# Kernel tuning notes

Hardware: AMD Instinct MI355X
Metric: run time of the kernel (lower is better)

The kernel has to match this reference:

```python
import jax, jax.numpy as jnp
import numpy as np

# Static module config (from Encoder's CropConv layers)
B, CIN, COUT, H, W = 32, 256, 256, 64, 64
K, STRIDE, PAD, DIL = 3, 2, 1, 1
OVERLAP, CENTER = 0, 4


def _build_crop_mask(in_h, out_h, out_w, center_size, overlap):
    """Faithful replica of CropConv's python-loop mask construction,
    including python-slice clamping to L = out_h*out_w."""
    L = out_h * out_w
    crop_start = (in_h - in_h // center_size) // 2 - overlap
    start_idx = in_h * crop_start + crop_start
    crop_size = in_h // center_size + overlap * 2
    not_cropped = crop_start * 2

    def seg_len(a, b):
        # length of python slice [a:b] on an array of length L
        return max(0, min(b, L) - min(a, L))

    segs = []
    for i in range(crop_size):
        if i == 0:
            segs.append(np.ones(seg_len(0, start_idx), bool))
        if i == crop_size - 1:
            segs.append(np.zeros(seg_len(start_idx, start_idx + crop_size), bool))
            segs.append(np.ones(seg_len(start_idx + crop_size, in_h * in_h), bool))
            break
        segs.append(np.zeros(seg_len(start_idx, start_idx + crop_size), bool))
        segs.append(np.ones(seg_len(start_idx + crop_size, start_idx + not_cropped), bool))
        start_idx += in_h
    mask = np.concatenate(segs)
    assert mask.shape[0] == L, (mask.shape[0], L)
    return mask.reshape(out_h, out_w)


def setup_inputs() -> dict:
    key = jax.random.key(0)
    kx, kw = jax.random.split(key)
    x = jax.random.normal(kx, (B, CIN, H, W), dtype=jnp.float32)
    # kaiming_normal(mode='fan_out', nonlinearity='relu'): std = sqrt(2 / (COUT*K*K))
    std = np.sqrt(2.0 / (COUT * K * K)).astype(np.float32)
    weight = jax.random.normal(kw, (COUT, CIN, K, K), dtype=jnp.float32) * std
    return {"x": x, "weight": weight}


def reference(x, weight):
    out_h = (H - K + 2 * PAD) // STRIDE + 1
    out_w = (W - K + 2 * PAD) // STRIDE + 1
    # unfold + matmul == standard convolution; use the efficient fused form
    out = jax.lax.conv_general_dilated(
        x, weight,
        window_strides=(STRIDE, STRIDE),
        padding=[(PAD, PAD), (PAD, PAD)],
        rhs_dilation=(DIL, DIL),
        dimension_numbers=("NCHW", "OIHW", "NCHW"))  # [B, COUT, out_h, out_w]
    mask = jnp.asarray(_build_crop_mask(H, out_h, out_w, CENTER, OVERLAP))
    return jnp.where(mask[None, None, :, :], out, jnp.float32(0.0))
```

## Files before the change

### kernel.cpp

```cpp
#include <hip/hip_runtime.h>


#define B_   32
#define CIN  256
#define COUT 256
#define H_   64
#define W_   64
#define OH   32
#define OW   32

typedef _Float16 f16;
typedef _Float16 half8 __attribute__((ext_vector_type(8)));
typedef float    floatx16 __attribute__((ext_vector_type(16)));

__global__ __launch_bounds__(256) void repack_w_kernel(const float* __restrict__ w,
                                                       f16* __restrict__ rp) {
  int o = blockIdx.x * 256 + threadIdx.x;
  int ci_l = o & 15;
  int tt = o >> 4;
  int co_l = tt & 127; tt >>= 7;
  int khw = tt % 9;    tt /= 9;
  int cc   = tt & 15;  tt >>= 4;
  int co_t = tt;
  int co = co_t * 128 + co_l;
  int ci = cc * 16 + ci_l;
  rp[o] = (f16)w[(co * CIN + ci) * 9 + khw];
}

static __device__ __forceinline__ void wg_barrier() {
  __builtin_amdgcn_sched_barrier(0);
  asm volatile("s_waitcnt lgkmcnt(0)" ::: "memory");
  __builtin_amdgcn_s_barrier();
  __builtin_amdgcn_sched_barrier(0);
}

__global__ __launch_bounds__(256, 2) void conv_mfma_kernel(
    const float* __restrict__ x, const f16* __restrict__ rp,
    float* __restrict__ out) {
  __shared__ __align__(16) f16 xs[19040];

  const int t    = threadIdx.x;
  const int lane = t & 63;
  const int wave = t >> 6;
  const int wm   = wave >> 1;
  const int wn   = wave & 1;

  const int blk  = blockIdx.x;
  const int b    = blk >> 4;
  const int rem  = blk & 15;
  const int co_t = rem >> 3;
  const int oh0  = (rem & 7) << 2;
  const int ih0  = 2 * oh0 - 1;

  const float* xb = x + (size_t)b * CIN * H_ * W_;

  const int iw  = t & 63;
  const int rru = __builtin_amdgcn_readfirstlane(t >> 6);
  const int k0  = (lane >> 5) * 8;
  const int ml  = lane & 31;
  const int p_st   = iw & 1;
  const int idx_st = (iw + p_st) >> 1;
  const int gx     = (idx_st >> 3) & 1;

  f16* const xs0 = xs;
  f16* const xs1 = xs + 9520;

  const f16* const AbL = rp + (size_t)co_t * (16 * 9 * 128 * 16)
                            + (wm * 64 + ml) * 16 + k0;

  floatx16 acc[2][2];
#pragma unroll
  for (int mi = 0; mi < 2; ++mi)
#pragma unroll
    for (int nj = 0; nj < 2; ++nj)
#pragma unroll
      for (int i = 0; i < 16; ++i) acc[mi][nj][i] = 0.f;

  float xv[3][2][8];

  auto load_x = [&](const float* bcc) {
#pragma unroll
    for (int it = 0; it < 3; ++it) {
      const int r = rru + it * 4;
      if (r < 9) {
        const int ih = ih0 + r;
        if (ih >= 0) {
          const float* p0 = bcc + (size_t)ih * 64 + iw;
#pragma unroll
          for (int g = 0; g < 2; ++g)
#pragma unroll
            for (int c = 0; c < 8; ++c)
              xv[it][g][c] = p0[(size_t)(g * 8 + c) * 4096];
        } else {
#pragma unroll
          for (int g = 0; g < 2; ++g)
#pragma unroll
            for (int c = 0; c < 8; ++c) xv[it][g][c] = 0.f;
        }
      }
    }
  };

  auto write_x = [&](f16* xoth) {
    f16* d = xoth + p_st * 4760 + idx_st * 16;
#pragma unroll
    for (int it = 0; it < 3; ++it) {
      const int r = rru + it * 4;
      if (r < 9) {
#pragma unroll
        for (int g = 0; g < 2; ++g) {
          half8 v;
#pragma unroll
          for (int c = 0; c < 8; ++c) v[c] = (f16)xv[it][g][c];
          *(half8*)&d[r * 528 + (g ^ gx) * 8] = v;
        }
      }
    }
  };

  auto compute = [&](const f16* Abc, const f16* xcur) {
    half8 a0[9], a1[9];
#pragma unroll
    for (int khw = 0; khw < 9; ++khw) {
      a0[khw] = *(const half8*)&Abc[khw * 2048];
      a1[khw] = *(const half8*)&Abc[khw * 2048 + 512];
    }
    const f16* Be  = xcur + wn * 2112 + ml * 16 + (k0 ^ (ml & 8));
    const f16* Bo1 = Be + 4760;
    const f16* Bo2 = xcur + 4760 + wn * 2112 + (ml + 1) * 16 + (k0 ^ ((ml + 1) & 8));
    __builtin_amdgcn_s_setprio(1);
#pragma unroll
    for (int kh = 0; kh < 3; ++kh) {
#pragma unroll
      for (int kw = 0; kw < 3; ++kw) {
        const int khw = kh * 3 + kw;
        const f16* Bp = (kw == 0) ? Bo1 : (kw == 1) ? Be : Bo2;
#pragma unroll
        for (int nj = 0; nj < 2; ++nj) {
          half8 bf = *(const half8*)&Bp[nj * 1056 + kh * 528];
          acc[0][nj] = __builtin_amdgcn_mfma_f32_32x32x16_f16(a0[khw], bf, acc[0][nj], 0, 0, 0);
          acc[1][nj] = __builtin_amdgcn_mfma_f32_32x32x16_f16(a1[khw], bf, acc[1][nj], 0, 0, 0);
        }
      }
    }
    __builtin_amdgcn_s_setprio(0);
  };

  if (t < 144) {
    const int r = t >> 4, ci = t & 15;
    xs0[4760 + r * 528 + ci] = (f16)0.f;
    xs1[4760 + r * 528 + ci] = (f16)0.f;
  }

  load_x(xb);
  write_x(xs0);
  load_x(xb + 65536);
  __syncthreads();

  const f16* Abc = AbL;
  f16* curp = xs0;
  f16* othp = xs1;
#pragma unroll 1
  for (int cc = 0; cc < 16; ++cc) {
    compute(Abc, curp);
    Abc += 18432;
    if (cc < 15) {
      write_x(othp);
      if (cc < 14) load_x(xb + (size_t)(cc + 2) * 65536);
      wg_barrier();
      f16* tm = curp; curp = othp; othp = tm;
    }
  }

  const int col = ml;
  const int rowbase = (lane >> 5) * 4;
  float* ob = out + ((size_t)b * COUT + co_t * 128 + wm * 64) * (OH * OW);
#pragma unroll
  for (int mi = 0; mi < 2; ++mi) {
#pragma unroll
    for (int nj = 0; nj < 2; ++nj) {
      const int oh = oh0 + wn * 2 + nj;
#pragma unroll
      for (int r = 0; r < 16; ++r) {
        const int row = mi * 32 + (r & 3) + 8 * (r >> 2) + rowbase;
        ob[(size_t)row * (OH * OW) + oh * OW + col] = acc[mi][nj][r];
      }
    }
  }
}

extern "C" void kernel_launch(void* const* d_in, const int* in_sizes, int n_in,
                              void* d_out, int out_size, void* d_ws, size_t ws_size,
                              hipStream_t stream) {
  const float* x = (const float*)d_in[0];
  const float* w = (const float*)d_in[1];
  float* out = (float*)d_out;
  f16* rp = (f16*)d_ws;

  repack_w_kernel<<<2304, 256, 0, stream>>>(w, rp);
  conv_mfma_kernel<<<512, 256, 0, stream>>>(x, rp, out);
}
```

Baseline: 227.9 us.

## Halve output-row tile per block to double grid and raise occupancy

Each block now covers 2 output rows instead of 4, so the grid doubles to 1024 blocks and the per-block LDS input tile shrinks. Accumulators drop to two MFMA tiles per wave, and the A fragments are loaded per kh instead of all nine up front. Launch bounds go to 4 blocks per CU. The aim is more resident waves to hide latency and better CU balance. The cost is reloading weight fragments for twice as many blocks, redundant input halo rows, and half the MFMA work per weight load.

```diff
diff --git a/kernel.cpp b/kernel.cpp
--- a/kernel.cpp
+++ b/kernel.cpp
@@ -34,10 +34,14 @@
   __builtin_amdgcn_sched_barrier(0);
 }
 
-__global__ __launch_bounds__(256, 2) void conv_mfma_kernel(
+#define PLANE 2640
+#define ODD   2648
+#define XBUF  5288
+
+__global__ __launch_bounds__(256, 4) void conv_mfma_kernel(
     const float* __restrict__ x, const f16* __restrict__ rp,
     float* __restrict__ out) {
-  __shared__ __align__(16) f16 xs[19040];
+  __shared__ __align__(16) f16 xs[2 * XBUF];
 
   const int t    = threadIdx.x;
   const int lane = t & 63;
@@ -46,110 +50,99 @@
   const int wn   = wave & 1;
 
   const int blk  = blockIdx.x;
-  const int b    = blk >> 4;
-  const int rem  = blk & 15;
-  const int co_t = rem >> 3;
-  const int oh0  = (rem & 7) << 2;
-  const int ih0  = 2 * oh0 - 1;
+  const int b    = blk >> 5;
+  const int rem  = blk & 31;
+  const int co_t = rem >> 4;
+  const int ohp  = rem & 15;
+  const int oh0  = ohp << 1;
+  const int ih0  = (ohp << 2) - 1;
 
   const float* xb = x + (size_t)b * CIN * H_ * W_;
 
-  const int iw  = t & 63;
-  const int rru = __builtin_amdgcn_readfirstlane(t >> 6);
-  const int k0  = (lane >> 5) * 8;
-  const int ml  = lane & 31;
+  const int iw    = t & 63;
+  const int g_st  = (t >> 6) & 1;
+  const int rbase = __builtin_amdgcn_readfirstlane(t >> 7) * 3;
+  const int k0 = (lane >> 5) * 8;
+  const int ml = lane & 31;
   const int p_st   = iw & 1;
   const int idx_st = (iw + p_st) >> 1;
   const int gx     = (idx_st >> 3) & 1;
 
   f16* const xs0 = xs;
-  f16* const xs1 = xs + 9520;
+  f16* const xs1 = xs + XBUF;
 
   const f16* const AbL = rp + (size_t)co_t * (16 * 9 * 128 * 16)
                             + (wm * 64 + ml) * 16 + k0;
 
-  floatx16 acc[2][2];
+  floatx16 acc[2];
 #pragma unroll
   for (int mi = 0; mi < 2; ++mi)
 #pragma unroll
-    for (int nj = 0; nj < 2; ++nj)
-#pragma unroll
-      for (int i = 0; i < 16; ++i) acc[mi][nj][i] = 0.f;
+    for (int i = 0; i < 16; ++i) acc[mi][i] = 0.f;
 
-  float xv[3][2][8];
+  float xv[3][8];
 
   auto load_x = [&](const float* bcc) {
 #pragma unroll
     for (int it = 0; it < 3; ++it) {
-      const int r = rru + it * 4;
-      if (r < 9) {
+      const int r = rbase + it;
+      if (r < 5) {
         const int ih = ih0 + r;
         if (ih >= 0) {
-          const float* p0 = bcc + (size_t)ih * 64 + iw;
+          const float* p0 = bcc + (size_t)(g_st * 8) * 4096 + (size_t)ih * 64 + iw;
 #pragma unroll
-          for (int g = 0; g < 2; ++g)
-#pragma unroll
-            for (int c = 0; c < 8; ++c)
-              xv[it][g][c] = p0[(size_t)(g * 8 + c) * 4096];
+          for (int c = 0; c < 8; ++c) xv[it][c] = p0[(size_t)c * 4096];
         } else {
 #pragma unroll
-          for (int g = 0; g < 2; ++g)
-#pragma unroll
-            for (int c = 0; c < 8; ++c) xv[it][g][c] = 0.f;
+          for (int c = 0; c < 8; ++c) xv[it][c] = 0.f;
         }
       }
     }
   };
 
   auto write_x = [&](f16* xoth) {
-    f16* d = xoth + p_st * 4760 + idx_st * 16;
+    f16* d = xoth + p_st * ODD + idx_st * 16 + (g_st ^ gx) * 8;
 #pragma unroll
     for (int it = 0; it < 3; ++it) {
-      const int r = rru + it * 4;
-      if (r < 9) {
+      const int r = rbase + it;
+      if (r < 5) {
+        half8 v;
 #pragma unroll
-        for (int g = 0; g < 2; ++g) {
-          half8 v;
-#pragma unroll
-          for (int c = 0; c < 8; ++c) v[c] = (f16)xv[it][g][c];
-          *(half8*)&d[r * 528 + (g ^ gx) * 8] = v;
-        }
+        for (int c = 0; c < 8; ++c) v[c] = (f16)xv[it][c];
+        *(half8*)&d[r * 528] = v;
       }
     }
   };
 
   auto compute = [&](const f16* Abc, const f16* xcur) {
-    half8 a0[9], a1[9];
-#pragma unroll
-    for (int khw = 0; khw < 9; ++khw) {
-      a0[khw] = *(const half8*)&Abc[khw * 2048];
-      a1[khw] = *(const half8*)&Abc[khw * 2048 + 512];
-    }
-    const f16* Be  = xcur + wn * 2112 + ml * 16 + (k0 ^ (ml & 8));
-    const f16* Bo1 = Be + 4760;
-    const f16* Bo2 = xcur + 4760 + wn * 2112 + (ml + 1) * 16 + (k0 ^ ((ml + 1) & 8));
+    const f16* Be  = xcur + wn * 1056 + ml * 16 + (k0 ^ (ml & 8));
+    const f16* Bo1 = Be + ODD;
+    const f16* Bo2 = xcur + ODD + wn * 1056 + (ml + 1) * 16 + (k0 ^ ((ml + 1) & 8));
     __builtin_amdgcn_s_setprio(1);
 #pragma unroll
     for (int kh = 0; kh < 3; ++kh) {
+      half8 a0[3], a1[3];
 #pragma unroll
       for (int kw = 0; kw < 3; ++kw) {
-        const int khw = kh * 3 + kw;
+        a0[kw] = *(const half8*)&Abc[(kh * 3 + kw) * 2048];
+        a1[kw] = *(const half8*)&Abc[(kh * 3 + kw) * 2048 + 512];
+      }
+#pragma unroll
+      for (int kw = 0; kw < 3; ++kw) {
         const f16* Bp = (kw == 0) ? Bo1 : (kw == 1) ? Be : Bo2;
-#pragma unroll
-        for (int nj = 0; nj < 2; ++nj) {
-          half8 bf = *(const half8*)&Bp[nj * 1056 + kh * 528];
-          acc[0][nj] = __builtin_amdgcn_mfma_f32_32x32x16_f16(a0[khw], bf, acc[0][nj], 0, 0, 0);
-          acc[1][nj] = __builtin_amdgcn_mfma_f32_32x32x16_f16(a1[khw], bf, acc[1][nj], 0, 0, 0);
-        }
+        half8 bf = *(const half8*)&Bp[kh * 528];
+        acc[0] = __builtin_amdgcn_mfma_f32_32x32x16_f16(a0[kw], bf, acc[0], 0, 0, 0);
+        acc[1] = __builtin_amdgcn_mfma_f32_32x32x16_f16(a1[kw], bf, acc[1], 0, 0, 0);
       }
     }
     __builtin_amdgcn_s_setprio(0);
   };
 
-  if (t < 144) {
-    const int r = t >> 4, ci = t & 15;
-    xs0[4760 + r * 528 + ci] = (f16)0.f;
-    xs1[4760 + r * 528 + ci] = (f16)0.f;
+  if (t < 160) {
+    const int bufi = t >= 80;
+    const int u = t - bufi * 80;
+    const int r = u >> 4, ci = u & 15;
+    xs[bufi * XBUF + ODD + r * 528 + ci] = (f16)0.f;
   }
 
   load_x(xb);
@@ -174,17 +167,15 @@
 
   const int col = ml;
   const int rowbase = (lane >> 5) * 4;
-  float* ob = out + ((size_t)b * COUT + co_t * 128 + wm * 64) * (OH * OW);
+  const int oh = oh0 + wn;
+  float* ob = out + ((size_t)b * COUT + co_t * 128 + wm * 64) * (OH * OW)
+                  + (size_t)oh * OW + col;
 #pragma unroll
   for (int mi = 0; mi < 2; ++mi) {
 #pragma unroll
-    for (int nj = 0; nj < 2; ++nj) {
-      const int oh = oh0 + wn * 2 + nj;
-#pragma unroll
-      for (int r = 0; r < 16; ++r) {
-        const int row = mi * 32 + (r & 3) + 8 * (r >> 2) + rowbase;
-        ob[(size_t)row * (OH * OW) + oh * OW + col] = acc[mi][nj][r];
-      }
+    for (int r = 0; r < 16; ++r) {
+      const int row = mi * 32 + (r & 3) + 8 * (r >> 2) + rowbase;
+      ob[(size_t)row * (OH * OW)] = acc[mi][r];
     }
   }
 }
@@ -198,5 +189,5 @@
   f16* rp = (f16*)d_ws;
 
   repack_w_kernel<<<2304, 256, 0, stream>>>(w, rp);
-  conv_mfma_kernel<<<512, 256, 0, stream>>>(x, rp, out);
+  conv_mfma_kernel<<<1024, 256, 0, stream>>>(x, rp, out);
 }
```

Measured after the change: 246.1 us. 8.0% more time.

## Process two input-channel chunks per pipeline stage to halve barriers

Applied to the files above, without the earlier changes.

Each main-loop iteration now covers two 16-channel chunks, so the x staging buffers in LDS are doubled and two register sets of prefetched x values are kept. This halves the number of workgroup barriers and loop iterations and puts more global loads in flight per stage. Weight fragments are now loaded per kernel row instead of all nine at once. In exchange, LDS use doubles to about 76 KB per block and register pressure rises from the second xv array, which could reduce occupancy below two blocks per CU or cause spills.

```diff
diff --git a/kernel.cpp b/kernel.cpp
--- a/kernel.cpp
+++ b/kernel.cpp
@@ -34,10 +34,13 @@
   __builtin_amdgcn_sched_barrier(0);
 }
 
+#define SUBT  9520
+#define XBUF  (2 * SUBT)
+
 __global__ __launch_bounds__(256, 2) void conv_mfma_kernel(
     const float* __restrict__ x, const f16* __restrict__ rp,
     float* __restrict__ out) {
-  __shared__ __align__(16) f16 xs[19040];
+  __shared__ __align__(16) f16 xs[2 * XBUF];
 
   const int t    = threadIdx.x;
   const int lane = t & 63;
@@ -63,7 +66,7 @@
   const int gx     = (idx_st >> 3) & 1;
 
   f16* const xs0 = xs;
-  f16* const xs1 = xs + 9520;
+  f16* const xs1 = xs + XBUF;
 
   const f16* const AbL = rp + (size_t)co_t * (16 * 9 * 128 * 16)
                             + (wm * 64 + ml) * 16 + k0;
@@ -76,9 +79,10 @@
 #pragma unroll
       for (int i = 0; i < 16; ++i) acc[mi][nj][i] = 0.f;
 
-  float xv[3][2][8];
-
-  auto load_x = [&](const float* bcc) {
+  float xva[3][2][8], xvb[3][2][8];
+
+  auto load_x = [&](float (&xv)[3][2][8], int cc16) {
+    const float* bcc = xb + (size_t)cc16 * 16 * 4096;
 #pragma unroll
     for (int it = 0; it < 3; ++it) {
       const int r = rru + it * 4;
@@ -101,8 +105,8 @@
     }
   };
 
-  auto write_x = [&](f16* xoth) {
-    f16* d = xoth + p_st * 4760 + idx_st * 16;
+  auto write_x = [&](float (&xv)[3][2][8], f16* xsub) {
+    f16* d = xsub + p_st * 4760 + idx_st * 16;
 #pragma unroll
     for (int it = 0; it < 3; ++it) {
       const int r = rru + it * 4;
@@ -119,27 +123,31 @@
   };
 
   auto compute = [&](const f16* Abc, const f16* xcur) {
-    half8 a0[9], a1[9];
-#pragma unroll
-    for (int khw = 0; khw < 9; ++khw) {
-      a0[khw] = *(const half8*)&Abc[khw * 2048];
-      a1[khw] = *(const half8*)&Abc[khw * 2048 + 512];
-    }
-    const f16* Be  = xcur + wn * 2112 + ml * 16 + (k0 ^ (ml & 8));
-    const f16* Bo1 = Be + 4760;
-    const f16* Bo2 = xcur + 4760 + wn * 2112 + (ml + 1) * 16 + (k0 ^ ((ml + 1) & 8));
     __builtin_amdgcn_s_setprio(1);
 #pragma unroll
-    for (int kh = 0; kh < 3; ++kh) {
-#pragma unroll
-      for (int kw = 0; kw < 3; ++kw) {
-        const int khw = kh * 3 + kw;
-        const f16* Bp = (kw == 0) ? Bo1 : (kw == 1) ? Be : Bo2;
-#pragma unroll
-        for (int nj = 0; nj < 2; ++nj) {
-          half8 bf = *(const half8*)&Bp[nj * 1056 + kh * 528];
-          acc[0][nj] = __builtin_amdgcn_mfma_f32_32x32x16_f16(a0[khw], bf, acc[0][nj], 0, 0, 0);
-          acc[1][nj] = __builtin_amdgcn_mfma_f32_32x32x16_f16(a1[khw], bf, acc[1][nj], 0, 0, 0);
+    for (int s = 0; s < 2; ++s) {
+      const f16* As  = Abc + s * 18432;
+      const f16* xss = xcur + s * SUBT;
+      const f16* Be  = xss + wn * 2112 + ml * 16 + (k0 ^ (ml & 8));
+      const f16* Bo1 = Be + 4760;
+      const f16* Bo2 = xss + 4760 + wn * 2112 + (ml + 1) * 16 + (k0 ^ ((ml + 1) & 8));
+#pragma unroll
+      for (int kh = 0; kh < 3; ++kh) {
+        half8 a0[3], a1[3];
+#pragma unroll
+        for (int kw = 0; kw < 3; ++kw) {
+          a0[kw] = *(const half8*)&As[(kh * 3 + kw) * 2048];
+          a1[kw] = *(const half8*)&As[(kh * 3 + kw) * 2048 + 512];
+        }
+#pragma unroll
+        for (int kw = 0; kw < 3; ++kw) {
+          const f16* Bp = (kw == 0) ? Bo1 : (kw == 1) ? Be : Bo2;
+#pragma unroll
+          for (int nj = 0; nj < 2; ++nj) {
+            half8 bf = *(const half8*)&Bp[nj * 1056 + kh * 528];
+            acc[0][nj] = __builtin_amdgcn_mfma_f32_32x32x16_f16(a0[kw], bf, acc[0][nj], 0, 0, 0);
+            acc[1][nj] = __builtin_amdgcn_mfma_f32_32x32x16_f16(a1[kw], bf, acc[1][nj], 0, 0, 0);
+          }
         }
       }
     }
@@ -148,25 +156,33 @@
 
   if (t < 144) {
     const int r = t >> 4, ci = t & 15;
-    xs0[4760 + r * 528 + ci] = (f16)0.f;
-    xs1[4760 + r * 528 + ci] = (f16)0.f;
+#pragma unroll
+    for (int sb = 0; sb < 4; ++sb)
+      xs[sb * SUBT + 4760 + r * 528 + ci] = (f16)0.f;
   }
 
-  load_x(xb);
-  write_x(xs0);
-  load_x(xb + 65536);
+  load_x(xva, 0);
+  load_x(xvb, 1);
+  write_x(xva, xs0);
+  write_x(xvb, xs0 + SUBT);
+  load_x(xva, 2);
+  load_x(xvb, 3);
   __syncthreads();
 
   const f16* Abc = AbL;
   f16* curp = xs0;
   f16* othp = xs1;
 #pragma unroll 1
-  for (int cc = 0; cc < 16; ++cc) {
+  for (int pi = 0; pi < 8; ++pi) {
     compute(Abc, curp);
-    Abc += 18432;
-    if (cc < 15) {
-      write_x(othp);
-      if (cc < 14) load_x(xb + (size_t)(cc + 2) * 65536);
+    Abc += 36864;
+    if (pi < 7) {
+      write_x(xva, othp);
+      write_x(xvb, othp + SUBT);
+      if (pi < 6) {
+        load_x(xva, 2 * pi + 4);
+        load_x(xvb, 2 * pi + 5);
+      }
       wg_barrier();
       f16* tm = curp; curp = othp; othp = tm;
     }
```

Measured after the change: 239.8 us. +5.2%, slower.
